# Optimization experiments

Hardware: AMD Instinct MI355X
Metric: run time of the kernel (lower is better)

## Reference

```python
import jax, jax.numpy as jnp
import numpy as np


def _lstm_cell(x, h, c, Wih, Whh, b):
    # torch gate order: input, forget, cell(g), output
    gates = x @ Wih.T + h @ Whh.T + b  # [B, 4H]
    i, f, g, o = jnp.split(gates, 4, axis=-1)
    i = jax.nn.sigmoid(i)
    f = jax.nn.sigmoid(f)
    g = jnp.tanh(g)
    o = jax.nn.sigmoid(o)
    c = f * c + i * g
    return o * jnp.tanh(c), c


def setup_inputs() -> dict:
    key = jax.random.key(0)
    ks = jax.random.split(key, 20)
    B, Te, Td, X, H = 4096, 168, 24, 8, 64
    s = 0.1  # weight scale for numerical sanity in the AR sampling loop
    return {
        "enc_x": jax.random.normal(ks[0], (B, Te, X), jnp.float32),
        "enc_z": jax.random.uniform(ks[1], (B, Te, 1), jnp.float32),
        "dec_x": jax.random.normal(ks[2], (B, Td, X - 1), jnp.float32),
        "v": jax.random.uniform(ks[3], (B, 1, 1), jnp.float32) + 0.5,  # positive scale
        "eps": jax.random.normal(ks[4], (B, Td, 1), jnp.float32),
        "W_ih0": s * jax.random.normal(ks[5], (4 * H, X), jnp.float32),
        "W_hh0": s * jax.random.normal(ks[6], (4 * H, H), jnp.float32),
        "b0": s * jax.random.normal(ks[7], (4 * H,), jnp.float32),
        "W_ih1": s * jax.random.normal(ks[8], (4 * H, H), jnp.float32),
        "W_hh1": s * jax.random.normal(ks[9], (4 * H, H), jnp.float32),
        "b1": s * jax.random.normal(ks[10], (4 * H,), jnp.float32),
        "W_ih2": s * jax.random.normal(ks[11], (4 * H, H), jnp.float32),
        "W_hh2": s * jax.random.normal(ks[12], (4 * H, H), jnp.float32),
        "b2": s * jax.random.normal(ks[13], (4 * H,), jnp.float32),
        "w_m": s * jax.random.normal(ks[14], (H, 1), jnp.float32),
        "b_m": jnp.zeros((1,), jnp.float32),
        "w_a": s * jax.random.normal(ks[15], (H, 1), jnp.float32),
        "b_a": jnp.zeros((1,), jnp.float32),
    }


def reference(enc_x, enc_z, dec_x, v, eps,
              W_ih0, W_hh0, b0, W_ih1, W_hh1, b1, W_ih2, W_hh2, b2,
              w_m, b_m, w_a, b_a):
    B = enc_x.shape[0]
    H = W_hh0.shape[1]

    def step3(x, h, c):
        h0, c0 = _lstm_cell(x, h[0], c[0], W_ih0, W_hh0, b0)
        h1, c1 = _lstm_cell(h0, h[1], c[1], W_ih1, W_hh1, b1)
        h2, c2 = _lstm_cell(h1, h[2], c[2], W_ih2, W_hh2, b2)
        return (h0, h1, h2), (c0, c1, c2), h2

    z0 = jnp.zeros((B, H), enc_x.dtype)
    h = (z0, z0, z0)
    c = (z0, z0, z0)

    # ---- encoder: 3-layer LSTM over Te steps ----
    def enc_step(carry, x_t):
        h, c = carry
        h, c, _ = step3(x_t, h, c)
        return (h, c), None

    (h, c), _ = jax.lax.scan(enc_step, (h, c), jnp.swapaxes(enc_x, 0, 1))

    vf = v[:, 0, :]                 # [B, 1]
    z = enc_z[:, -1, :] / vf        # [B, 1]

    def dec_step(carry, inp):
        h, c, z = carry
        x_t, e_t = inp              # [B, X-1], [B, 1]
        x = jnp.concatenate([z, x_t], axis=-1)   # [B, X]
        h, c, o = step3(x, h, c)
        m = (o @ w_m + b_m) * vf                  # Gaussian mean, rescaled
        a = jax.nn.softplus(o @ w_a + b_a) * vf   # Gaussian std, rescaled
        zs = m + a * e_t                          # reparameterized sample
        return (h, c, zs / vf), zs

    xs = (jnp.swapaxes(dec_x, 0, 1), jnp.swapaxes(eps, 0, 1))
    _, Z = jax.lax.scan(dec_step, (h, c, z), xs)  # [Td, B, 1]
    return jnp.swapaxes(Z, 0, 1)                  # [B, Td, 1]
```

## Files before the change

kernel.cpp:

```cpp
#include <hip/hip_runtime.h>
#include <math.h>

#define B_TOT 4096
#define TE 168
#define TD 24
#define NWG 256
#define HSTR 72

typedef _Float16 f16;
typedef __attribute__((ext_vector_type(8))) _Float16 f16x8;
typedef __attribute__((ext_vector_type(4))) float f32x4;

#define SCL_S (-1.4426950408889634f)
#define SCL_G (2.885390081777927f)

__global__ __launch_bounds__(256) void pack_kernel(
    const float* __restrict__ Wih0, const float* __restrict__ Whh0,
    const float* __restrict__ Wih1, const float* __restrict__ Whh1,
    const float* __restrict__ Wih2, const float* __restrict__ Whh2,
    f16* __restrict__ pk)
{
    int idx = blockIdx.x * 256 + threadIdx.x;
    int j = idx & 7;
    int t = idx >> 3;
    int ln = t & 63; t >>= 6;
    int c  = t & 3;  t >>= 2;
    int q  = t & 3;  t >>= 2;
    int l  = t % 3;
    int w  = t / 3;
    int row = q * 64 + w * 16 + (ln & 15);
    int k   = c * 32 + ((ln >> 4) << 3) + j;
    float val = 0.f;
    if (l == 0) {
        if (k < 8)                 val = Wih0[row * 8 + k];
        else if (k >= 32 && k < 96) val = Whh0[row * 64 + (k - 32)];
    } else if (l == 1) {
        val = (k < 64) ? Wih1[row * 64 + k] : Whh1[row * 64 + (k - 64)];
    } else {
        val = (k < 64) ? Wih2[row * 64 + k] : Whh2[row * 64 + (k - 64)];
    }
    const float sc = (q == 2) ? SCL_G : SCL_S;
    pk[idx] = (f16)(val * sc);
}

__device__ __forceinline__ float softplusf(float x) { return fmaxf(x, 0.f) + log1pf(__expf(-fabsf(x))); }

__global__ __launch_bounds__(512, 2) void lstm_kernel(
    const float* __restrict__ enc_x, const float* __restrict__ enc_z,
    const float* __restrict__ dec_x, const float* __restrict__ v,
    const float* __restrict__ eps,   const f16* __restrict__ pk,
    const float* __restrict__ b0, const float* __restrict__ b1,
    const float* __restrict__ b2,
    const float* __restrict__ w_m, const float* __restrict__ b_m,
    const float* __restrict__ w_a, const float* __restrict__ b_a,
    float* __restrict__ out)
{
    const int tid  = threadIdx.x;
    const int lane = tid & 63;
    const int wv   = (tid >> 6) & 3;
    const int half = tid >> 8;
    const int bg   = blockIdx.x * 16;
    const int m16  = lane & 15;
    const int quad = lane >> 4;

    __shared__ f16  hbuf[2][3][16][HSTR];
    __shared__ f16  xbuf[2][16][32];
    __shared__ float zbuf[16];

    {
        uint* hz = (uint*)&hbuf[0][0][0][0];
        const int HW = 2 * 3 * 16 * HSTR / 2;
        for (int i = tid; i < HW; i += 512) hz[i] = 0u;
        ((uint*)&xbuf[0][0][0])[tid] = 0u;
    }

    f16x8 wgt[7][4];
#define PKOFF(l, q, c) ((((((size_t)wv * 3 + (l)) * 4 + (q)) * 4 + (c)) * 64 + lane) * 8)
    if (half == 0) {
#pragma unroll
        for (int q = 0; q < 4; ++q) {
#pragma unroll
            for (int c = 0; c < 3; ++c) wgt[c][q]     = *(const f16x8*)(pk + PKOFF(0, q, c));
#pragma unroll
            for (int c = 0; c < 4; ++c) wgt[3 + c][q] = *(const f16x8*)(pk + PKOFF(1, q, c));
        }
    } else {
#pragma unroll
        for (int q = 0; q < 4; ++q)
#pragma unroll
            for (int c = 0; c < 4; ++c) wgt[c][q] = *(const f16x8*)(pk + PKOFF(2, q, c));
    }
#undef PKOFF

    const int hid_self = wv * 16 + m16;
    float bsc[2][4];
#pragma unroll
    for (int q = 0; q < 4; ++q) {
        const float sc = (q == 2) ? SCL_G : SCL_S;
        if (half == 0) {
            bsc[0][q] = b0[q * 64 + hid_self] * sc;
            bsc[1][q] = b1[q * 64 + hid_self] * sc;
        } else {
            bsc[0][q] = b2[q * 64 + hid_self] * sc;
            bsc[1][q] = 0.f;
        }
    }

    f16* hb = &hbuf[0][0][0][0];
    const int aoff = m16 * HSTR + quad * 8;
    float cst[2][4] = {};
    const f32x4 zc = {0.f, 0.f, 0.f, 0.f};

#define HBASE(pp, l) (hb + ((pp) * 3 + (l)) * (16 * HSTR))
#define MFMA16(af, bf, cf) __builtin_amdgcn_mfma_f32_16x16x32_f16(af, bf, cf, 0, 0, 0)

#define MM_F(P, aptr, wi)                                                     \
    {                                                                         \
        f16x8 af = *(const f16x8*)(aptr);                                     \
        P##0 = MFMA16(af, wgt[wi][0], zc);                                    \
        P##1 = MFMA16(af, wgt[wi][1], zc);                                    \
        P##2 = MFMA16(af, wgt[wi][2], zc);                                    \
        P##3 = MFMA16(af, wgt[wi][3], zc);                                    \
    }
#define MM(P, aptr, wi)                                                       \
    {                                                                         \
        f16x8 af = *(const f16x8*)(aptr);                                     \
        P##0 = MFMA16(af, wgt[wi][0], P##0);                                  \
        P##1 = MFMA16(af, wgt[wi][1], P##1);                                  \
        P##2 = MFMA16(af, wgt[wi][2], P##2);                                  \
        P##3 = MFMA16(af, wgt[wi][3], P##3);                                  \
    }

#define CELL(P, li, lh, PP)                                                   \
    {                                                                         \
        f16* hw = HBASE(PP, lh) + hid_self;                                   \
        _Pragma("unroll")                                                     \
        for (int r = 0; r < 4; ++r) {                                         \
            float Ei = __builtin_amdgcn_exp2f(P##0[r] + bsc[li][0]);          \
            float Ef = __builtin_amdgcn_exp2f(P##1[r] + bsc[li][1]);          \
            float Eg = __builtin_amdgcn_exp2f(P##2[r] + bsc[li][2]);          \
            float Eo = __builtin_amdgcn_exp2f(P##3[r] + bsc[li][3]);          \
            float ef1 = 1.f + Ef;                                             \
            float pig = (1.f + Ei) * (1.f + Eg);                              \
            float R   = __builtin_amdgcn_rcpf(pig * ef1);                     \
            float fv  = pig * R;                                              \
            float ig  = (Eg - 1.f) * ef1 * R;                                 \
            float cn  = fmaf(fv, cst[li][r], ig);                             \
            cst[li][r] = cn;                                                  \
            float Ec  = __builtin_amdgcn_exp2f(cn * SCL_G);                   \
            float Roc = __builtin_amdgcn_rcpf((1.f + Eo) * (1.f + Ec));       \
            hw[(quad * 4 + r) * HSTR] = (f16)((Ec - 1.f) * Roc);              \
        }                                                                     \
    }

    const int  sidx = tid - 256;
    const bool isst = (sidx >= 0) && (sidx < 128);
    const int  mS = (sidx >> 3) & 15, kS = sidx & 7;
    const float* xrow = enc_x + ((size_t)(bg + mS) * TE) * 8 + kS;

#define ROUND(PP, D0, D1, D2, DS, DP, T0)                                     \
    {                                                                         \
        __syncthreads();                                                      \
        f32x4 ac0, ac1, ac2, ac3, bc0, bc1, bc2, bc3;                         \
        if (half == 0) {                                                      \
            if (D0) { MM_F(ac, &xbuf[PP][0][0] + m16 * 32 + quad * 8, 0); }   \
            if (D1) { MM_F(bc, HBASE(1 - (PP), 0) + aoff, 3); }               \
            if (D0) { MM(ac, HBASE(1 - (PP), 0) + aoff,      1); }            \
            if (D1) { MM(bc, HBASE(1 - (PP), 0) + aoff + 32, 4); }            \
            if (D0) { MM(ac, HBASE(1 - (PP), 0) + aoff + 32, 2); }            \
            if (D1) { MM(bc, HBASE(1 - (PP), 1) + aoff,      5);              \
                      MM(bc, HBASE(1 - (PP), 1) + aoff + 32, 6); }            \
            if (D0) CELL(ac, 0, 0, PP);                                       \
            if (D1) CELL(bc, 1, 1, PP);                                       \
        } else {                                                              \
            if (D2) { MM_F(ac, HBASE(1 - (PP), 1) + aoff,      0);            \
                      MM(ac, HBASE(1 - (PP), 1) + aoff + 32, 1);              \
                      MM(ac, HBASE(1 - (PP), 2) + aoff,      2);              \
                      MM(ac, HBASE(1 - (PP), 2) + aoff + 32, 3); }            \
            if (DS && isst) {                                                 \
                xbuf[1 - (PP)][mS][kS] = (f16)xpre;                           \
                if (DP) xpre = xrow[((T0) + 2) * 8];                          \
            }                                                                 \
            if (D2) CELL(ac, 0, 2, PP);                                       \
        }                                                                     \
    }

    __syncthreads();

    float xpre = 0.f;
    if (isst) {
        xbuf[0][mS][kS] = (f16)xrow[0];
        xpre = xrow[8];
    }
    ROUND(0, 1, 0, 0, 1, 1, 0)
    ROUND(1, 1, 1, 0, 1, 1, 1)
    for (int t = 2; t < 166; t += 2) {
        ROUND(0, 1, 1, 1, 1, 1, t)
        ROUND(1, 1, 1, 1, 1, 1, t + 1)
    }
    ROUND(0, 1, 1, 1, 1, 0, 166)
    ROUND(1, 1, 1, 1, 0, 0, 167)
    ROUND(0, 0, 1, 1, 0, 0, 168)
    ROUND(1, 0, 0, 1, 0, 0, 169)

    const int   mH = tid >> 4;
    const float vf = (half == 0) ? v[bg + mH] : 0.f;
    float wmr[4], war[4];
#pragma unroll
    for (int r = 0; r < 4; ++r) {
        wmr[r] = w_m[(tid & 15) + 16 * r];
        war[r] = w_a[(tid & 15) + 16 * r];
    }
    const float bmv = b_m[0], bav = b_a[0];
    if (half == 0 && (tid & 15) == 0)
        zbuf[mH] = enc_z[(size_t)(bg + mH) * TE + (TE - 1)] / vf;

#define DEC_STEP(PA, t)                                                       \
    {                                                                         \
        __syncthreads();                           \
        if (isst) {                                                           \
            float xv = (kS == 0) ? zbuf[mS]                                   \
                                 : dec_x[((size_t)(bg + mS) * TD + (t)) * 7 + (kS - 1)]; \
            xbuf[PA][mS][kS] = (f16)xv;                                       \
        }                                                                     \
        __syncthreads();                                       \
        f32x4 ac0, ac1, ac2, ac3;                                             \
        if (half == 0) {                                                      \
            MM_F(ac, &xbuf[PA][0][0] + m16 * 32 + quad * 8, 0);               \
            MM(ac, HBASE(1 - (PA), 0) + aoff,      1);                        \
            MM(ac, HBASE(1 - (PA), 0) + aoff + 32, 2);                        \
            CELL(ac, 0, 0, PA);                                               \
        }                                                                     \
        __syncthreads();                                  \
        if (half == 0) {                                                      \
            MM_F(ac, HBASE(PA, 0) + aoff,      3);                            \
            MM(ac, HBASE(PA, 0) + aoff + 32, 4);                              \
            MM(ac, HBASE(PA, 1) + aoff,      5);                              \
            MM(ac, HBASE(PA, 1) + aoff + 32, 6);                              \
            CELL(ac, 1, 1, 1 - (PA));                                         \
        }                                                                     \
        __syncthreads();                                \
        if (half == 1) {                                                      \
            MM_F(ac, HBASE(1 - (PA), 1) + aoff,      0);                      \
            MM(ac, HBASE(1 - (PA), 1) + aoff + 32, 1);                        \
            MM(ac, HBASE(1 - (PA), 2) + aoff,      2);                        \
            MM(ac, HBASE(1 - (PA), 2) + aoff + 32, 3);                        \
            CELL(ac, 0, 2, PA);                                               \
        }                                                                     \
        __syncthreads();                                  \
        if (half == 0) {                                                      \
            float sm = 0.f, sa = 0.f;                                         \
            const f16* h2p = HBASE(PA, 2) + mH * HSTR;                        \
            _Pragma("unroll")                                                 \
            for (int r = 0; r < 4; ++r) {                                     \
                float hv = (float)h2p[(tid & 15) + 16 * r];                   \
                sm += hv * wmr[r];                                            \
                sa += hv * war[r];                                            \
            }                                                                 \
            _Pragma("unroll")                                                 \
            for (int off = 1; off < 16; off <<= 1) {                          \
                sm += __shfl_xor(sm, off, 64);                                \
                sa += __shfl_xor(sa, off, 64);                                \
            }                                                                 \
            if ((tid & 15) == 0) {                                            \
                float mo  = (sm + bmv) * vf;                                  \
                float ao  = softplusf(sa + bav) * vf;                         \
                float zsv = mo + ao * eps[(size_t)(bg + mH) * TD + (t)];      \
                out[(size_t)(bg + mH) * TD + (t)] = zsv;                      \
                zbuf[mH] = zsv / vf;                                          \
            }                                                                 \
        }                                                                     \
    }

    for (int t = 0; t < TD; t += 2) {
        DEC_STEP(0, t)
        DEC_STEP(1, t + 1)
    }

#undef HBASE
#undef MFMA16
#undef MM_F
#undef MM
#undef CELL
#undef ROUND
#undef DEC_STEP
}

extern "C" void kernel_launch(void* const* d_in, const int* in_sizes, int n_in,
                              void* d_out, int out_size, void* d_ws, size_t ws_size,
                              hipStream_t stream) {
    const float* enc_x = (const float*)d_in[0];
    const float* enc_z = (const float*)d_in[1];
    const float* dec_x = (const float*)d_in[2];
    const float* v     = (const float*)d_in[3];
    const float* eps   = (const float*)d_in[4];
    const float* Wih0  = (const float*)d_in[5];
    const float* Whh0  = (const float*)d_in[6];
    const float* b0    = (const float*)d_in[7];
    const float* Wih1  = (const float*)d_in[8];
    const float* Whh1  = (const float*)d_in[9];
    const float* b1    = (const float*)d_in[10];
    const float* Wih2  = (const float*)d_in[11];
    const float* Whh2  = (const float*)d_in[12];
    const float* b2    = (const float*)d_in[13];
    const float* w_m   = (const float*)d_in[14];
    const float* b_m   = (const float*)d_in[15];
    const float* w_a   = (const float*)d_in[16];
    const float* b_a   = (const float*)d_in[17];
    float* out = (float*)d_out;
    f16*   pk  = (f16*)d_ws;

    pack_kernel<<<384, 256, 0, stream>>>(Wih0, Whh0, Wih1, Whh1, Wih2, Whh2, pk);
    lstm_kernel<<<NWG, 512, 0, stream>>>(enc_x, enc_z, dec_x, v, eps, pk,
                                         b0, b1, b2, w_m, b_m, w_a, b_a, out);
}
```

Measured before the change: 326.4 us.

## Split three LSTM layers across three wave groups and fold bias into MFMA accumulator

Grows the workgroup from 512 to 768 threads so each LSTM layer gets its own group of four waves, instead of one group handling layers 0 and 1 and another handling layer 2. This evens out the per-round critical path, which was set by the group doing two layers of matmul and cell work. The bias is now used as the initial MFMA accumulator rather than added in the gate math, and each group holds fewer weight registers. In exchange, more waves per workgroup raise register and scheduling pressure, and the launch bounds change to allow 3 blocks per unit.

```diff
diff --git a/kernel.cpp b/kernel.cpp
--- a/kernel.cpp
+++ b/kernel.cpp
@@ -45,7 +45,7 @@
 
 __device__ __forceinline__ float softplusf(float x) { return fmaxf(x, 0.f) + log1pf(__expf(-fabsf(x))); }
 
-__global__ __launch_bounds__(512, 2) void lstm_kernel(
+__global__ __launch_bounds__(768, 3) void lstm_kernel(
     const float* __restrict__ enc_x, const float* __restrict__ enc_z,
     const float* __restrict__ dec_x, const float* __restrict__ v,
     const float* __restrict__ eps,   const f16* __restrict__ pk,
@@ -58,7 +58,7 @@
     const int tid  = threadIdx.x;
     const int lane = tid & 63;
     const int wv   = (tid >> 6) & 3;
-    const int half = tid >> 8;
+    const int role = tid >> 8;
     const int bg   = blockIdx.x * 16;
     const int m16  = lane & 15;
     const int quad = lane >> 4;
@@ -70,46 +70,37 @@
     {
         uint* hz = (uint*)&hbuf[0][0][0][0];
         const int HW = 2 * 3 * 16 * HSTR / 2;
-        for (int i = tid; i < HW; i += 512) hz[i] = 0u;
-        ((uint*)&xbuf[0][0][0])[tid] = 0u;
-    }
-
-    f16x8 wgt[7][4];
+        for (int i = tid; i < HW; i += 768) hz[i] = 0u;
+        uint* xz = (uint*)&xbuf[0][0][0];
+        for (int i = tid; i < 512; i += 768) xz[i] = 0u;
+    }
+
+    f16x8 wgt[4][4];
 #define PKOFF(l, q, c) ((((((size_t)wv * 3 + (l)) * 4 + (q)) * 4 + (c)) * 64 + lane) * 8)
-    if (half == 0) {
+    {
+        const int nch = (role == 0) ? 3 : 4;
+#pragma unroll
+        for (int q = 0; q < 4; ++q)
+            for (int c = 0; c < nch; ++c)
+                wgt[c][q] = *(const f16x8*)(pk + PKOFF(role, q, c));
+    }
+#undef PKOFF
+
+    const int hid_self = wv * 16 + m16;
+    f32x4 bsp[4];
+    {
+        const float* bp = (role == 0) ? b0 : (role == 1) ? b1 : b2;
 #pragma unroll
         for (int q = 0; q < 4; ++q) {
-#pragma unroll
-            for (int c = 0; c < 3; ++c) wgt[c][q]     = *(const f16x8*)(pk + PKOFF(0, q, c));
-#pragma unroll
-            for (int c = 0; c < 4; ++c) wgt[3 + c][q] = *(const f16x8*)(pk + PKOFF(1, q, c));
-        }
-    } else {
-#pragma unroll
-        for (int q = 0; q < 4; ++q)
-#pragma unroll
-            for (int c = 0; c < 4; ++c) wgt[c][q] = *(const f16x8*)(pk + PKOFF(2, q, c));
-    }
-#undef PKOFF
-
-    const int hid_self = wv * 16 + m16;
-    float bsc[2][4];
-#pragma unroll
-    for (int q = 0; q < 4; ++q) {
-        const float sc = (q == 2) ? SCL_G : SCL_S;
-        if (half == 0) {
-            bsc[0][q] = b0[q * 64 + hid_self] * sc;
-            bsc[1][q] = b1[q * 64 + hid_self] * sc;
-        } else {
-            bsc[0][q] = b2[q * 64 + hid_self] * sc;
-            bsc[1][q] = 0.f;
+            const float sc = (q == 2) ? SCL_G : SCL_S;
+            float bv = bp[q * 64 + hid_self] * sc;
+            bsp[q] = (f32x4){bv, bv, bv, bv};
         }
     }
 
     f16* hb = &hbuf[0][0][0][0];
     const int aoff = m16 * HSTR + quad * 8;
-    float cst[2][4] = {};
-    const f32x4 zc = {0.f, 0.f, 0.f, 0.f};
+    float cst[4] = {};
 
 #define HBASE(pp, l) (hb + ((pp) * 3 + (l)) * (16 * HSTR))
 #define MFMA16(af, bf, cf) __builtin_amdgcn_mfma_f32_16x16x32_f16(af, bf, cf, 0, 0, 0)
@@ -117,10 +108,10 @@
 #define MM_F(P, aptr, wi)                                                     \
     {                                                                         \
         f16x8 af = *(const f16x8*)(aptr);                                     \
-        P##0 = MFMA16(af, wgt[wi][0], zc);                                    \
-        P##1 = MFMA16(af, wgt[wi][1], zc);                                    \
-        P##2 = MFMA16(af, wgt[wi][2], zc);                                    \
-        P##3 = MFMA16(af, wgt[wi][3], zc);                                    \
+        P##0 = MFMA16(af, wgt[wi][0], bsp[0]);                                \
+        P##1 = MFMA16(af, wgt[wi][1], bsp[1]);                                \
+        P##2 = MFMA16(af, wgt[wi][2], bsp[2]);                                \
+        P##3 = MFMA16(af, wgt[wi][3], bsp[3]);                                \
     }
 #define MM(P, aptr, wi)                                                       \
     {                                                                         \
@@ -131,29 +122,29 @@
         P##3 = MFMA16(af, wgt[wi][3], P##3);                                  \
     }
 
-#define CELL(P, li, lh, PP)                                                   \
+#define CELL(P, lh, PP)                                                       \
     {                                                                         \
         f16* hw = HBASE(PP, lh) + hid_self;                                   \
         _Pragma("unroll")                                                     \
         for (int r = 0; r < 4; ++r) {                                         \
-            float Ei = __builtin_amdgcn_exp2f(P##0[r] + bsc[li][0]);          \
-            float Ef = __builtin_amdgcn_exp2f(P##1[r] + bsc[li][1]);          \
-            float Eg = __builtin_amdgcn_exp2f(P##2[r] + bsc[li][2]);          \
-            float Eo = __builtin_amdgcn_exp2f(P##3[r] + bsc[li][3]);          \
+            float Ei = __builtin_amdgcn_exp2f(P##0[r]);                       \
+            float Ef = __builtin_amdgcn_exp2f(P##1[r]);                       \
+            float Eg = __builtin_amdgcn_exp2f(P##2[r]);                       \
+            float Eo = __builtin_amdgcn_exp2f(P##3[r]);                       \
             float ef1 = 1.f + Ef;                                             \
             float pig = (1.f + Ei) * (1.f + Eg);                              \
             float R   = __builtin_amdgcn_rcpf(pig * ef1);                     \
             float fv  = pig * R;                                              \
             float ig  = (Eg - 1.f) * ef1 * R;                                 \
-            float cn  = fmaf(fv, cst[li][r], ig);                             \
-            cst[li][r] = cn;                                                  \
+            float cn  = fmaf(fv, cst[r], ig);                                 \
+            cst[r] = cn;                                                      \
             float Ec  = __builtin_amdgcn_exp2f(cn * SCL_G);                   \
             float Roc = __builtin_amdgcn_rcpf((1.f + Eo) * (1.f + Ec));       \
             hw[(quad * 4 + r) * HSTR] = (f16)((Ec - 1.f) * Roc);              \
         }                                                                     \
     }
 
-    const int  sidx = tid - 256;
+    const int  sidx = tid - 512;
     const bool isst = (sidx >= 0) && (sidx < 128);
     const int  mS = (sidx >> 3) & 15, kS = sidx & 7;
     const float* xrow = enc_x + ((size_t)(bg + mS) * TE) * 8 + kS;
@@ -161,27 +152,34 @@
 #define ROUND(PP, D0, D1, D2, DS, DP, T0)                                     \
     {                                                                         \
         __syncthreads();                                                      \
-        f32x4 ac0, ac1, ac2, ac3, bc0, bc1, bc2, bc3;                         \
-        if (half == 0) {                                                      \
-            if (D0) { MM_F(ac, &xbuf[PP][0][0] + m16 * 32 + quad * 8, 0); }   \
-            if (D1) { MM_F(bc, HBASE(1 - (PP), 0) + aoff, 3); }               \
-            if (D0) { MM(ac, HBASE(1 - (PP), 0) + aoff,      1); }            \
-            if (D1) { MM(bc, HBASE(1 - (PP), 0) + aoff + 32, 4); }            \
-            if (D0) { MM(ac, HBASE(1 - (PP), 0) + aoff + 32, 2); }            \
-            if (D1) { MM(bc, HBASE(1 - (PP), 1) + aoff,      5);              \
-                      MM(bc, HBASE(1 - (PP), 1) + aoff + 32, 6); }            \
-            if (D0) CELL(ac, 0, 0, PP);                                       \
-            if (D1) CELL(bc, 1, 1, PP);                                       \
+        f32x4 a0, a1, a2, a3;                                                 \
+        if (role == 0) {                                                      \
+            if (D0) {                                                         \
+                MM_F(a, &xbuf[PP][0][0] + m16 * 32 + quad * 8, 0);            \
+                MM(a, HBASE(1 - (PP), 0) + aoff,      1);                     \
+                MM(a, HBASE(1 - (PP), 0) + aoff + 32, 2);                     \
+                CELL(a, 0, PP);                                               \
+            }                                                                 \
+        } else if (role == 1) {                                               \
+            if (D1) {                                                         \
+                MM_F(a, HBASE(1 - (PP), 0) + aoff,      0);                   \
+                MM(a, HBASE(1 - (PP), 0) + aoff + 32, 1);                     \
+                MM(a, HBASE(1 - (PP), 1) + aoff,      2);                     \
+                MM(a, HBASE(1 - (PP), 1) + aoff + 32, 3);                     \
+                CELL(a, 1, PP);                                               \
+            }                                                                 \
         } else {                                                              \
-            if (D2) { MM_F(ac, HBASE(1 - (PP), 1) + aoff,      0);            \
-                      MM(ac, HBASE(1 - (PP), 1) + aoff + 32, 1);              \
-                      MM(ac, HBASE(1 - (PP), 2) + aoff,      2);              \
-                      MM(ac, HBASE(1 - (PP), 2) + aoff + 32, 3); }            \
+            if (D2) {                                                         \
+                MM_F(a, HBASE(1 - (PP), 1) + aoff,      0);                   \
+                MM(a, HBASE(1 - (PP), 1) + aoff + 32, 1);                     \
+                MM(a, HBASE(1 - (PP), 2) + aoff,      2);                     \
+                MM(a, HBASE(1 - (PP), 2) + aoff + 32, 3);                     \
+            }                                                                 \
             if (DS && isst) {                                                 \
                 xbuf[1 - (PP)][mS][kS] = (f16)xpre;                           \
                 if (DP) xpre = xrow[((T0) + 2) * 8];                          \
             }                                                                 \
-            if (D2) CELL(ac, 0, 2, PP);                                       \
+            if (D2) CELL(a, 2, PP);                                           \
         }                                                                     \
     }
 
@@ -203,8 +201,8 @@
     ROUND(0, 0, 1, 1, 0, 0, 168)
     ROUND(1, 0, 0, 1, 0, 0, 169)
 
-    const int   mH = tid >> 4;
-    const float vf = (half == 0) ? v[bg + mH] : 0.f;
+    const int   mH = (tid >> 4) & 15;
+    const float vf = (role == 0) ? v[bg + mH] : 0.f;
     float wmr[4], war[4];
 #pragma unroll
     for (int r = 0; r < 4; ++r) {
@@ -212,7 +210,7 @@
         war[r] = w_a[(tid & 15) + 16 * r];
     }
     const float bmv = b_m[0], bav = b_a[0];
-    if (half == 0 && (tid & 15) == 0)
+    if (role == 0 && (tid & 15) == 0)
         zbuf[mH] = enc_z[(size_t)(bg + mH) * TE + (TE - 1)] / vf;
 
 #define DEC_STEP(PA, t)                                                       \
@@ -224,31 +222,31 @@
             xbuf[PA][mS][kS] = (f16)xv;                                       \
         }                                                                     \
         __syncthreads();                                       \
-        f32x4 ac0, ac1, ac2, ac3;                                             \
-        if (half == 0) {                                                      \
-            MM_F(ac, &xbuf[PA][0][0] + m16 * 32 + quad * 8, 0);               \
-            MM(ac, HBASE(1 - (PA), 0) + aoff,      1);                        \
-            MM(ac, HBASE(1 - (PA), 0) + aoff + 32, 2);                        \
-            CELL(ac, 0, 0, PA);                                               \
+        f32x4 a0, a1, a2, a3;                                                 \
+        if (role == 0) {                                                      \
+            MM_F(a, &xbuf[PA][0][0] + m16 * 32 + quad * 8, 0);                \
+            MM(a, HBASE(1 - (PA), 0) + aoff,      1);                         \
+            MM(a, HBASE(1 - (PA), 0) + aoff + 32, 2);                         \
+            CELL(a, 0, PA);                                                   \
         }                                                                     \
         __syncthreads();                                  \
-        if (half == 0) {                                                      \
-            MM_F(ac, HBASE(PA, 0) + aoff,      3);                            \
-            MM(ac, HBASE(PA, 0) + aoff + 32, 4);                              \
-            MM(ac, HBASE(PA, 1) + aoff,      5);                              \
-            MM(ac, HBASE(PA, 1) + aoff + 32, 6);                              \
-            CELL(ac, 1, 1, 1 - (PA));                                         \
+        if (role == 1) {                                                      \
+            MM_F(a, HBASE(PA, 0) + aoff,      0);                             \
+            MM(a, HBASE(PA, 0) + aoff + 32, 1);                               \
+            MM(a, HBASE(PA, 1) + aoff,      2);                               \
+            MM(a, HBASE(PA, 1) + aoff + 32, 3);                               \
+            CELL(a, 1, 1 - (PA));                                             \
         }                                                                     \
         __syncthreads();                                \
-        if (half == 1) {                                                      \
-            MM_F(ac, HBASE(1 - (PA), 1) + aoff,      0);                      \
-            MM(ac, HBASE(1 - (PA), 1) + aoff + 32, 1);                        \
-            MM(ac, HBASE(1 - (PA), 2) + aoff,      2);                        \
-            MM(ac, HBASE(1 - (PA), 2) + aoff + 32, 3);                        \
-            CELL(ac, 0, 2, PA);                                               \
+        if (role == 2) {                                                      \
+            MM_F(a, HBASE(1 - (PA), 1) + aoff,      0);                       \
+            MM(a, HBASE(1 - (PA), 1) + aoff + 32, 1);                         \
+            MM(a, HBASE(1 - (PA), 2) + aoff,      2);                         \
+            MM(a, HBASE(1 - (PA), 2) + aoff + 32, 3);                         \
+            CELL(a, 2, PA);                                                   \
         }                                                                     \
         __syncthreads();                                  \
-        if (half == 0) {                                                      \
+        if (role == 0) {                                                      \
             float sm = 0.f, sa = 0.f;                                         \
             const f16* h2p = HBASE(PA, 2) + mH * HSTR;                        \
             _Pragma("unroll")                                                 \
@@ -311,6 +309,6 @@
     f16*   pk  = (f16*)d_ws;
 
     pack_kernel<<<384, 256, 0, stream>>>(Wih0, Whh0, Wih1, Whh1, Wih2, Whh2, pk);
-    lstm_kernel<<<NWG, 512, 0, stream>>>(enc_x, enc_z, dec_x, v, eps, pk,
+    lstm_kernel<<<NWG, 768, 0, stream>>>(enc_x, enc_z, dec_x, v, eps, pk,
                                          b0, b1, b2, w_m, b_m, w_a, b_a, out);
 }
```

Measured after the change: 1.281 ms. 292% more time.
